# Performance work log

Measured on AMD Instinct MI355X. Metric: run time of the kernel, lower is better.

The kernel has to match this reference:

```python
import jax, jax.numpy as jnp
import numpy as np

N = 100000   # nodes (single ntype)
R = 3        # relations
E = 500000   # edges per relation
H = 4        # attention heads
F = 64       # out_feat per head
IN = 256     # in_feat
NEG_SLOPE = 0.2  # DGL GATConv default


def setup_inputs() -> dict:
    key = jax.random.key(0)
    ks = jax.random.split(key, 7)
    x = jax.random.normal(ks[0], (N, IN), jnp.float32)
    src = jax.random.randint(ks[1], (R, E), 0, N, dtype=jnp.int32)
    dst = jax.random.randint(ks[2], (R, E), 0, N, dtype=jnp.int32)
    W = jax.random.normal(ks[3], (R, IN, H * F), jnp.float32) / np.sqrt(IN).astype(np.float32)
    attn_l = jax.random.normal(ks[4], (R, H, F), jnp.float32) * 0.1
    attn_r = jax.random.normal(ks[5], (R, H, F), jnp.float32) * 0.1
    bias = jnp.zeros((R, H * F), jnp.float32)
    return {"x": x, "W": W, "attn_l": attn_l, "attn_r": attn_r, "bias": bias,
            "src": src, "dst": dst}


def _gat_relation(x, W_r, al_r, ar_r, b_r, src_r, dst_r):
    # projection: [N, H, F]
    z = (x @ W_r).reshape(N, H, F)
    # per-node attention logits: [N, H]
    el = jnp.sum(z * al_r, axis=-1)
    er = jnp.sum(z * ar_r, axis=-1)
    # edge scores: [E, H]
    e = jax.nn.leaky_relu(el[src_r] + er[dst_r], negative_slope=NEG_SLOPE)
    # segment softmax over incoming edges of each dst node
    m = jax.ops.segment_max(e, dst_r, num_segments=N)      # [N, H]
    ee = jnp.exp(e - m[dst_r])                              # [E, H]
    den = jax.ops.segment_sum(ee, dst_r, num_segments=N)   # [N, H]
    alpha = ee / den[dst_r]                                 # [E, H]
    # weighted scatter-aggregate: [N, H, F]
    rst = jax.ops.segment_sum(z[src_r] * alpha[:, :, None], dst_r, num_segments=N)
    return rst + b_r.reshape(1, H, F)


def reference(x, W, attn_l, attn_r, bias, src, dst):
    # HeteroGraphConv aggregates relations targeting the same ntype with 'sum'
    out = jnp.zeros((N, H, F), x.dtype)
    for r in range(R):
        out = out + _gat_relation(x, W[r], attn_l[r], attn_r[r], bias[r], src[r], dst[r])
    # RelGATConvLayer._apply: activation(h.view(-1, out_feat*num_heads)); dropout=0
    return jax.nn.elu(out.reshape(N, H * F))
```

## Files before the change

### kernel.cpp

```cpp
#include <hip/hip_runtime.h>
#include <hip/hip_bf16.h>


#define RN 100000
#define RE 500000
#define RH 4
#define RIN 256
#define RR 3
#define RHF 256
#define NE3 (RR * RE)
#define N3  (RR * RN)

typedef __attribute__((ext_vector_type(8))) short short8;
typedef __attribute__((ext_vector_type(4))) float f32x4;

static __device__ __forceinline__ float b2f(unsigned short u) {
  return __uint_as_float(((unsigned int)u) << 16);
}
static __device__ __forceinline__ unsigned short f2b(float f) {
  unsigned int u = __float_as_uint(f);
  u += 0x7FFF + ((u >> 16) & 1);
  return (unsigned short)(u >> 16);
}

__global__ __launch_bounds__(256) void rgat_convx(
    const float* __restrict__ x, unsigned short* __restrict__ xb) {
  const size_t i = ((size_t)blockIdx.x * 256 + threadIdx.x) * 4;
  if (i >= (size_t)RN * RIN) return;
  const float4 v = *(const float4*)(x + i);
  ushort4 o;
  o.x = f2b(v.x); o.y = f2b(v.y); o.z = f2b(v.z); o.w = f2b(v.w);
  *(ushort4*)(xb + i) = o;
}

__global__ __launch_bounds__(256) void rgat_convw(
    const float* __restrict__ W, unsigned short* __restrict__ wbt) {
  const int o = blockIdx.x * 256 + threadIdx.x;
  if (o >= RR * RIN * RHF) return;
  const int r = o / (RIN * RHF);
  const int rem = o - r * (RIN * RHF);
  const int n = rem >> 8;
  const int k = rem & 255;
  wbt[o] = f2b(W[r * (RIN * RHF) + k * RHF + n]);
}

__global__ __launch_bounds__(256) void rgat_gemm_bf16(
    const unsigned short* __restrict__ xb, const unsigned short* __restrict__ wbt,
    unsigned short* __restrict__ zb, const float* __restrict__ al,
    const float* __restrict__ ar, float* __restrict__ el,
    float* __restrict__ er) {
  __shared__ unsigned short As[128 * 32];
  __shared__ unsigned short Bs[128 * 32];
  const int tid = threadIdx.x;
  const int lane = tid & 63, wid = tid >> 6;
  const int wr = wid >> 1, wc = wid & 1;
  const int m0 = blockIdx.x * 128;
  const int n0 = blockIdx.y * 128;
  const int r  = blockIdx.z;

  f32x4 acc[4][4] = {};
  const unsigned short* Bbase = wbt + (size_t)r * (RIN * RHF);

  for (int k0 = 0; k0 < RIN; k0 += 32) {
#pragma unroll
    for (int i = 0; i < 2; ++i) {
      const int c = wid * 128 + i * 64 + lane;
      const int row = c >> 2, c4 = c & 3;
      const unsigned short* ga = xb + (size_t)(m0 + row) * RIN + k0 + c4 * 8;
      __builtin_amdgcn_global_load_lds(
          (const __attribute__((address_space(1))) void*)ga,
          (__attribute__((address_space(3))) void*)(As + (wid * 128 + i * 64) * 8),
          16, 0, 0);
      const unsigned short* gb = Bbase + (size_t)(n0 + row) * RIN + k0 + c4 * 8;
      __builtin_amdgcn_global_load_lds(
          (const __attribute__((address_space(1))) void*)gb,
          (__attribute__((address_space(3))) void*)(Bs + (wid * 128 + i * 64) * 8),
          16, 0, 0);
    }
    asm volatile("s_waitcnt vmcnt(0)" ::: "memory");
    __syncthreads();

    short8 af[4], bfr[4];
#pragma unroll
    for (int mi = 0; mi < 4; ++mi)
      af[mi] = *(const short8*)(As + ((wr * 64 + mi * 16 + (lane & 15)) * 32 + (lane >> 4) * 8));
#pragma unroll
    for (int ni = 0; ni < 4; ++ni)
      bfr[ni] = *(const short8*)(Bs + ((wc * 64 + ni * 16 + (lane & 15)) * 32 + (lane >> 4) * 8));
#pragma unroll
    for (int mi = 0; mi < 4; ++mi)
#pragma unroll
      for (int ni = 0; ni < 4; ++ni)
        acc[mi][ni] = __builtin_amdgcn_mfma_f32_16x16x32_bf16(af[mi], bfr[ni], acc[mi][ni], 0, 0, 0);
    __syncthreads();
  }

  const int head = blockIdx.y * 2 + wc;
  float alv[4], arv[4];
#pragma unroll
  for (int ni = 0; ni < 4; ++ni) {
    alv[ni] = al[r * RHF + head * 64 + ni * 16 + (lane & 15)];
    arv[ni] = ar[r * RHF + head * 64 + ni * 16 + (lane & 15)];
  }

  const int mbase = m0 + wr * 64;
#pragma unroll
  for (int mi = 0; mi < 4; ++mi) {
#pragma unroll
    for (int q = 0; q < 4; ++q) {
      const int m = mbase + mi * 16 + (lane >> 4) * 4 + q;
      float pl = 0.f, pr = 0.f;
#pragma unroll
      for (int ni = 0; ni < 4; ++ni) {
        pl += acc[mi][ni][q] * alv[ni];
        pr += acc[mi][ni][q] * arv[ni];
      }
#pragma unroll
      for (int off = 1; off < 16; off <<= 1) {
        pl += __shfl_xor(pl, off);
        pr += __shfl_xor(pr, off);
      }
      if (m < RN) {
        if ((lane & 15) == 0) {
          el[(size_t)(r * (size_t)RN + m) * RH + head] = pl;
          er[(size_t)(r * (size_t)RN + m) * RH + head] = pr;
        }
        unsigned short* zrow = zb + (size_t)r * ((size_t)RN * RHF) + (size_t)m * RHF
                               + n0 + wc * 64 + (lane & 15);
#pragma unroll
        for (int ni = 0; ni < 4; ++ni) zrow[ni * 16] = f2b(acc[mi][ni][q]);
      }
    }
  }
}

__global__ __launch_bounds__(256) void rgat_hist(
    const int* __restrict__ dst, int* __restrict__ deg2) {
  const int i = blockIdx.x * 256 + threadIdx.x;
  if (i >= NE3) return;
  const int r = i / RE;
  atomicAdd(&deg2[dst[i] * RR + r], 1);
}

__global__ __launch_bounds__(256) void rgat_scan1(
    const int* __restrict__ deg, int* __restrict__ offs, int* __restrict__ bsum) {
  __shared__ int sh[256];
  const int tid = threadIdx.x;
  const int base = blockIdx.x * 1024 + tid * 4;
  int v[4]; int s = 0;
#pragma unroll
  for (int j = 0; j < 4; ++j) {
    v[j] = (base + j < N3) ? deg[base + j] : 0;
    s += v[j];
  }
  sh[tid] = s;
  __syncthreads();
  for (int off = 1; off < 256; off <<= 1) {
    int t = (tid >= off) ? sh[tid - off] : 0;
    __syncthreads();
    sh[tid] += t;
    __syncthreads();
  }
  int run = sh[tid] - s;
  if (tid == 255) bsum[blockIdx.x] = sh[255];
#pragma unroll
  for (int j = 0; j < 4; ++j) {
    if (base + j < N3) offs[base + j] = run;
    run += v[j];
  }
}

__global__ __launch_bounds__(512) void rgat_scan2(int* __restrict__ bsum, int nb) {
  __shared__ int sh[512];
  const int tid = threadIdx.x;
  const int v = (tid < nb) ? bsum[tid] : 0;
  sh[tid] = v;
  __syncthreads();
  for (int off = 1; off < 512; off <<= 1) {
    int t = (tid >= off) ? sh[tid - off] : 0;
    __syncthreads();
    sh[tid] += t;
    __syncthreads();
  }
  if (tid < nb) bsum[tid] = sh[tid] - v;
}

__global__ __launch_bounds__(256) void rgat_scan3(
    int* __restrict__ offs, const int* __restrict__ bsum) {
  const int base = blockIdx.x * 1024 + threadIdx.x * 4;
  const int b = bsum[blockIdx.x];
#pragma unroll
  for (int j = 0; j < 4; ++j)
    if (base + j < N3) offs[base + j] += b;
}

__global__ __launch_bounds__(256) void rgat_scatter(
    const int* __restrict__ src, const int* __restrict__ dst,
    const float* __restrict__ el, const float* __restrict__ er,
    int* __restrict__ offs2, int* __restrict__ csrc,
    float4* __restrict__ cee) {
  const int i = blockIdx.x * 256 + threadIdx.x;
  if (i >= NE3) return;
  const int r = i / RE;
  const int s = src[i];
  const int d = dst[i];
  const int pos = atomicAdd(&offs2[d * RR + r], 1);
  const float4 elv = *(const float4*)(el + (size_t)(r * (size_t)RN + s) * RH);
  const float4 erv = *(const float4*)(er + (size_t)(r * (size_t)RN + d) * RH);
  float e0 = elv.x + erv.x, e1 = elv.y + erv.y, e2 = elv.z + erv.z, e3 = elv.w + erv.w;
  e0 = e0 > 0.f ? e0 : 0.2f * e0;
  e1 = e1 > 0.f ? e1 : 0.2f * e1;
  e2 = e2 > 0.f ? e2 : 0.2f * e2;
  e3 = e3 > 0.f ? e3 : 0.2f * e3;
  csrc[pos] = s;
  cee[pos] = make_float4(__expf(e0), __expf(e1), __expf(e2), __expf(e3));
}

__global__ __launch_bounds__(256) void rgat_den(
    const float4* __restrict__ cee, const int* __restrict__ deg2,
    const int* __restrict__ offs2, float* __restrict__ invd) {
  const int key = blockIdx.x * 256 + threadIdx.x;
  if (key >= N3) return;
  const int d = deg2[key];
  const int end = offs2[key];
  float s0 = 0.f, s1 = 0.f, s2 = 0.f, s3 = 0.f;
  for (int p = end - d; p < end; ++p) {
    const float4 v = cee[p];
    s0 += v.x; s1 += v.y; s2 += v.z; s3 += v.w;
  }
  float4 o;
  o.x = s0 > 0.f ? 1.f / s0 : 0.f;
  o.y = s1 > 0.f ? 1.f / s1 : 0.f;
  o.z = s2 > 0.f ? 1.f / s2 : 0.f;
  o.w = s3 > 0.f ? 1.f / s3 : 0.f;
  *(float4*)(invd + (size_t)key * RH) = o;
}

__global__ __launch_bounds__(256) void rgat_aggregate(
    const unsigned short* __restrict__ zb, const int* __restrict__ csrc,
    const float* __restrict__ ceef, const int* __restrict__ deg2,
    const int* __restrict__ offs2, const float* __restrict__ invd,
    const float* __restrict__ bias, float* __restrict__ out) {
  __shared__ float shn[4][RHF];
  const int n = blockIdx.x;
  const int tid = threadIdx.x;
  const int wid = tid >> 6, lane = tid & 63;
  const int hw = lane >> 5;
  const int sub = lane & 31;
  const int h = sub >> 3;
  const int c = sub * 8;

  float acc[8] = {};

#pragma unroll
  for (int r = 0; r < RR; ++r) {
    const int key = n * RR + r;
    const int dr = deg2[key];
    const int start = offs2[key] - dr;
    const float inv = invd[(size_t)key * RH + h];
    const unsigned short* zB = zb + (size_t)r * ((size_t)RN * RHF) + c;
    for (int base = wid * 8; base < dr; base += 32) {
      int ss[4]; float aa[4];
#pragma unroll
      for (int j = 0; j < 4; ++j) {
        const int t = base + j * 2 + hw;
        if (t < dr) {
          const int p = start + t;
          ss[j] = csrc[p];
          aa[j] = ceef[p * 4 + h];
        } else {
          ss[j] = 0;
          aa[j] = 0.f;
        }
      }
      short8 zv[4];
#pragma unroll
      for (int j = 0; j < 4; ++j)
        zv[j] = *(const short8*)(zB + (size_t)ss[j] * RHF);
#pragma unroll
      for (int j = 0; j < 4; ++j) {
        const float a = aa[j] * inv;
#pragma unroll
        for (int k = 0; k < 8; ++k)
          acc[k] += a * b2f((unsigned short)zv[j][k]);
      }
    }
  }

#pragma unroll
  for (int k = 0; k < 8; ++k) acc[k] += __shfl_xor(acc[k], 32);

  if (lane < 32) {
    *(float4*)&shn[wid][c]     = make_float4(acc[0], acc[1], acc[2], acc[3]);
    *(float4*)&shn[wid][c + 4] = make_float4(acc[4], acc[5], acc[6], acc[7]);
  }
  __syncthreads();

  const int col = tid;
  float v = shn[0][col] + shn[1][col] + shn[2][col] + shn[3][col]
          + bias[col] + bias[RHF + col] + bias[2 * RHF + col];
  v = v > 0.f ? v : (__expf(v) - 1.f);
  out[(size_t)n * RHF + col] = v;
}

extern "C" void kernel_launch(void* const* d_in, const int* in_sizes, int n_in,
                              void* d_out, int out_size, void* d_ws, size_t ws_size,
                              hipStream_t stream) {
  const float* x    = (const float*)d_in[0];
  const float* W    = (const float*)d_in[1];
  const float* al   = (const float*)d_in[2];
  const float* ar   = (const float*)d_in[3];
  const float* bias = (const float*)d_in[4];
  const int*   src  = (const int*)d_in[5];
  const int*   dst  = (const int*)d_in[6];
  float* out = (float*)d_out;

  char* p = (char*)d_ws;
  unsigned short* xb  = (unsigned short*)p; p += (size_t)RN * RIN * 2;
  unsigned short* wbt = (unsigned short*)p; p += (size_t)RR * RIN * RHF * 2;
  unsigned short* zb  = (unsigned short*)p; p += (size_t)RR * RN * RHF * 2;
  float* el    = (float*)p;  p += (size_t)RR * RN * RH * 4;
  float* er    = (float*)p;  p += (size_t)RR * RN * RH * 4;
  int* deg2    = (int*)p;    p += (size_t)N3 * 4;
  float* invd  = (float*)p;  p += (size_t)N3 * RH * 4;
  int* offs2   = (int*)p;    p += (size_t)N3 * 4;
  int* csrc    = (int*)p;    p += (size_t)NE3 * 4;
  float4* cee  = (float4*)p; p += (size_t)NE3 * 16;
  int* bsum    = (int*)p;    p += 2048;

  const int NB1 = (N3 + 1023) / 1024;

  hipMemsetAsync(deg2, 0, (size_t)N3 * 4, stream);

  rgat_convx<<<(RN * RIN / 4 + 255) / 256, 256, 0, stream>>>(x, xb);
  rgat_convw<<<(RR * RIN * RHF + 255) / 256, 256, 0, stream>>>(W, wbt);

  rgat_hist<<<(NE3 + 255) / 256, 256, 0, stream>>>(dst, deg2);
  rgat_scan1<<<NB1, 256, 0, stream>>>(deg2, offs2, bsum);
  rgat_scan2<<<1, 512, 0, stream>>>(bsum, NB1);
  rgat_scan3<<<NB1, 256, 0, stream>>>(offs2, bsum);

  rgat_gemm_bf16<<<dim3((RN + 127) / 128, RHF / 128, RR), 256, 0, stream>>>(
      xb, wbt, zb, al, ar, el, er);

  rgat_scatter<<<(NE3 + 255) / 256, 256, 0, stream>>>(src, dst, el, er, offs2,
                                                      csrc, cee);

  rgat_den<<<(N3 + 255) / 256, 256, 0, stream>>>(cee, deg2, offs2, invd);

  rgat_aggregate<<<RN, 256, 0, stream>>>(zb, csrc, (const float*)cee, deg2,
                                         offs2, invd, bias, out);
}
```

Baseline: 740.8 us.

## Merge per-relation edge loops into one flat loop with prenormalized alpha

The scatter now stores a combined row offset (relation*N + src), so the aggregate kernel treats the three relations' contiguous CSR segments for a node as one edge range. That range is split across 8 half-wave groups, two edges per group per iteration, which removes the per-relation loop overhead and the tail waste of handling each small segment separately. The softmax denominator kernel now rewrites cee in place as normalized alpha, so aggregate no longer loads invd, at the cost of a second read-write pass over cee. Fewer loads are in flight per iteration (2 instead of 4 per thread), which may reduce memory-level parallelism.

```diff
diff --git a/kernel.cpp b/kernel.cpp
--- a/kernel.cpp
+++ b/kernel.cpp
@@ -197,7 +197,7 @@
 __global__ __launch_bounds__(256) void rgat_scatter(
     const int* __restrict__ src, const int* __restrict__ dst,
     const float* __restrict__ el, const float* __restrict__ er,
-    int* __restrict__ offs2, int* __restrict__ csrc,
+    int* __restrict__ offs2, int* __restrict__ czoff,
     float4* __restrict__ cee) {
   const int i = blockIdx.x * 256 + threadIdx.x;
   if (i >= NE3) return;
@@ -212,13 +212,13 @@
   e1 = e1 > 0.f ? e1 : 0.2f * e1;
   e2 = e2 > 0.f ? e2 : 0.2f * e2;
   e3 = e3 > 0.f ? e3 : 0.2f * e3;
-  csrc[pos] = s;
+  czoff[pos] = r * RN + s;
   cee[pos] = make_float4(__expf(e0), __expf(e1), __expf(e2), __expf(e3));
 }
 
-__global__ __launch_bounds__(256) void rgat_den(
-    const float4* __restrict__ cee, const int* __restrict__ deg2,
-    const int* __restrict__ offs2, float* __restrict__ invd) {
+__global__ __launch_bounds__(256) void rgat_norm(
+    float4* __restrict__ cee, const int* __restrict__ deg2,
+    const int* __restrict__ offs2) {
   const int key = blockIdx.x * 256 + threadIdx.x;
   if (key >= N3) return;
   const int d = deg2[key];
@@ -228,62 +228,60 @@
     const float4 v = cee[p];
     s0 += v.x; s1 += v.y; s2 += v.z; s3 += v.w;
   }
-  float4 o;
-  o.x = s0 > 0.f ? 1.f / s0 : 0.f;
-  o.y = s1 > 0.f ? 1.f / s1 : 0.f;
-  o.z = s2 > 0.f ? 1.f / s2 : 0.f;
-  o.w = s3 > 0.f ? 1.f / s3 : 0.f;
-  *(float4*)(invd + (size_t)key * RH) = o;
+  const float i0 = s0 > 0.f ? 1.f / s0 : 0.f;
+  const float i1 = s1 > 0.f ? 1.f / s1 : 0.f;
+  const float i2 = s2 > 0.f ? 1.f / s2 : 0.f;
+  const float i3 = s3 > 0.f ? 1.f / s3 : 0.f;
+  for (int p = end - d; p < end; ++p) {
+    float4 v = cee[p];
+    v.x *= i0; v.y *= i1; v.z *= i2; v.w *= i3;
+    cee[p] = v;
+  }
 }
 
 __global__ __launch_bounds__(256) void rgat_aggregate(
-    const unsigned short* __restrict__ zb, const int* __restrict__ csrc,
-    const float* __restrict__ ceef, const int* __restrict__ deg2,
-    const int* __restrict__ offs2, const float* __restrict__ invd,
-    const float* __restrict__ bias, float* __restrict__ out) {
+    const unsigned short* __restrict__ zb, const int* __restrict__ czoff,
+    const float* __restrict__ alpha, const int* __restrict__ deg2,
+    const int* __restrict__ offs2, const float* __restrict__ bias,
+    float* __restrict__ out) {
   __shared__ float shn[4][RHF];
   const int n = blockIdx.x;
   const int tid = threadIdx.x;
   const int wid = tid >> 6, lane = tid & 63;
   const int hw = lane >> 5;
   const int sub = lane & 31;
+  const int hwid = wid * 2 + hw;
   const int h = sub >> 3;
   const int c = sub * 8;
 
+  const int k0 = n * RR;
+  const int start = offs2[k0] - deg2[k0];
+  const int dm = offs2[k0 + 2] - start;
+
   float acc[8] = {};
-
-#pragma unroll
-  for (int r = 0; r < RR; ++r) {
-    const int key = n * RR + r;
-    const int dr = deg2[key];
-    const int start = offs2[key] - dr;
-    const float inv = invd[(size_t)key * RH + h];
-    const unsigned short* zB = zb + (size_t)r * ((size_t)RN * RHF) + c;
-    for (int base = wid * 8; base < dr; base += 32) {
-      int ss[4]; float aa[4];
-#pragma unroll
-      for (int j = 0; j < 4; ++j) {
-        const int t = base + j * 2 + hw;
-        if (t < dr) {
-          const int p = start + t;
-          ss[j] = csrc[p];
-          aa[j] = ceef[p * 4 + h];
-        } else {
-          ss[j] = 0;
-          aa[j] = 0.f;
-        }
-      }
-      short8 zv[4];
-#pragma unroll
-      for (int j = 0; j < 4; ++j)
-        zv[j] = *(const short8*)(zB + (size_t)ss[j] * RHF);
-#pragma unroll
-      for (int j = 0; j < 4; ++j) {
-        const float a = aa[j] * inv;
-#pragma unroll
-        for (int k = 0; k < 8; ++k)
-          acc[k] += a * b2f((unsigned short)zv[j][k]);
-      }
+  const unsigned short* zB = zb + c;
+
+  for (int base = 0; base < dm; base += 16) {
+    int ss[2]; float aa[2];
+#pragma unroll
+    for (int j = 0; j < 2; ++j) {
+      const int t = base + j * 8 + hwid;
+      const int tc = t < dm ? t : dm - 1;
+      const int p = start + tc;
+      ss[j] = czoff[p];
+      const float af = alpha[p * 4 + h];
+      aa[j] = t < dm ? af : 0.f;
+    }
+    short8 zv[2];
+#pragma unroll
+    for (int j = 0; j < 2; ++j)
+      zv[j] = *(const short8*)(zB + (size_t)ss[j] * RHF);
+#pragma unroll
+    for (int j = 0; j < 2; ++j) {
+      const float a = aa[j];
+#pragma unroll
+      for (int k = 0; k < 8; ++k)
+        acc[k] += a * b2f((unsigned short)zv[j][k]);
     }
   }
 
@@ -322,9 +320,8 @@
   float* el    = (float*)p;  p += (size_t)RR * RN * RH * 4;
   float* er    = (float*)p;  p += (size_t)RR * RN * RH * 4;
   int* deg2    = (int*)p;    p += (size_t)N3 * 4;
-  float* invd  = (float*)p;  p += (size_t)N3 * RH * 4;
   int* offs2   = (int*)p;    p += (size_t)N3 * 4;
-  int* csrc    = (int*)p;    p += (size_t)NE3 * 4;
+  int* czoff   = (int*)p;    p += (size_t)NE3 * 4;
   float4* cee  = (float4*)p; p += (size_t)NE3 * 16;
   int* bsum    = (int*)p;    p += 2048;
 
@@ -344,10 +341,10 @@
       xb, wbt, zb, al, ar, el, er);
 
   rgat_scatter<<<(NE3 + 255) / 256, 256, 0, stream>>>(src, dst, el, er, offs2,
-                                                      csrc, cee);
-
-  rgat_den<<<(N3 + 255) / 256, 256, 0, stream>>>(cee, deg2, offs2, invd);
-
-  rgat_aggregate<<<RN, 256, 0, stream>>>(zb, csrc, (const float*)cee, deg2,
-                                         offs2, invd, bias, out);
-}
+                                                      czoff, cee);
+
+  rgat_norm<<<(N3 + 255) / 256, 256, 0, stream>>>(cee, deg2, offs2);
+
+  rgat_aggregate<<<RN, 256, 0, stream>>>(zb, czoff, (const float*)cee, deg2,
+                                         offs2, bias, out);
+}
```

After: 619.2 us. -16.4%, faster.
